# Kernel optimization log

Measured on AMD Instinct MI355X. Metric: run time of the kernel, lower is better.

Reference implementation:

```python
import jax, jax.numpy as jnp
import numpy as np

N_NODES = 100000
N_EDGES = 3200000
D_IN = 256
D_OUT = 256


def setup_inputs() -> dict:
    key = jax.random.key(0)
    k1, k2, k3, k4, k5 = jax.random.split(key, 5)
    inputs = jax.random.normal(k1, (N_NODES, D_IN), dtype=jnp.float32)
    adj_row = jax.random.randint(k2, (N_EDGES,), 0, N_NODES, dtype=jnp.int32)
    adj_col = jax.random.randint(k3, (N_EDGES,), 0, N_NODES, dtype=jnp.int32)
    adj_val = jax.random.uniform(k4, (N_EDGES,), dtype=jnp.float32)
    # xavier-uniform init for weight, zeros for bias (as in reset_parameters)
    limit = float(np.sqrt(6.0 / (D_IN + D_OUT)))
    weight = jax.random.uniform(k5, (D_IN, D_OUT), dtype=jnp.float32,
                                minval=-limit, maxval=limit)
    bias = jnp.zeros((D_OUT,), dtype=jnp.float32)
    return {"inputs": inputs, "adj_row": adj_row, "adj_col": adj_col,
            "adj_val": adj_val, "weight": weight, "bias": bias}


def reference(inputs, adj_row, adj_col, adj_val, weight, bias) -> jnp.ndarray:
    # support = X @ W  -> [N, D_OUT]
    support = inputs @ weight
    # SpMM: out[r] = sum_{e: row[e]==r} val[e] * support[col[e]]
    gathered = support[adj_col] * adj_val[:, None]          # [E, D_OUT]
    output = jax.ops.segment_sum(gathered, adj_row, num_segments=N_NODES)
    return output + bias
```

## Files before the change

### kernel.cpp

```cpp
#include <hip/hip_runtime.h>

#define N_NODES 100000
#define N_EDGES 3200000
#define D 256
#define GEMM_TILES (N_NODES / 32)
#define GEMM_BLOCKS ((GEMM_TILES + 3) / 4)
#define WSH_BLOCKS 32

#define RPB 16
#define NB_BUCKETS (N_NODES / RPB)
#define NBLK_B ((NB_BUCKETS + 255) / 256)
#define P2_CAP 4096

#define HIST_P 256
#define EDGES_PER_HB (N_EDGES / HIST_P)

using u16 = unsigned short;
using u32 = unsigned int;

typedef __attribute__((ext_vector_type(8))) short bf16x8;
typedef __attribute__((ext_vector_type(4))) float f32x4;

__device__ inline u16 f2bf(float f) {
    u32 x = __builtin_bit_cast(u32, f);
    return (u16)((x + 0x7FFFu + ((x >> 16) & 1u)) >> 16);
}
__device__ inline float bf2f(u16 u) {
    return __builtin_bit_cast(float, (u32)u << 16);
}

__global__ __launch_bounds__(256) void prep_kernel(
    const float* __restrict__ W, u16* __restrict__ Wf)
{
    const int t = blockIdx.x * 256 + threadIdx.x;
    const int kt = t >> 10;
    const int nt = (t >> 6) & 15;
    const int lane = t & 63;
    const int kbase = kt * 32 + ((lane >> 4) * 8);
    const int n = nt * 16 + (lane & 15);
    u16 frag[8];
    #pragma unroll
    for (int j = 0; j < 8; ++j)
        frag[j] = f2bf(W[(size_t)(kbase + j) * D + n]);
    #pragma unroll
    for (int j = 0; j < 8; ++j)
        Wf[(size_t)t * 8 + j] = frag[j];
}

__global__ __launch_bounds__(256) void gemm_kernel(
    const float* __restrict__ X, const u16* __restrict__ Wf,
    u16* __restrict__ S)
{
    const int lane = threadIdx.x & 63;
    const int tile = blockIdx.x * 4 + (threadIdx.x >> 6);
    if (tile >= GEMM_TILES) return;
    const int row0 = tile * 32;
    const int m = lane & 15;
    const int quad = lane >> 4;

    f32x4 acc0[16], acc1[16];
    #pragma unroll
    for (int t = 0; t < 16; ++t) {
        acc0[t] = (f32x4){0.f, 0.f, 0.f, 0.f};
        acc1[t] = (f32x4){0.f, 0.f, 0.f, 0.f};
    }

    const float* xA = X + (size_t)(row0 + m) * D + quad * 8;
    const float* xB = X + (size_t)(row0 + 16 + m) * D + quad * 8;
    const bf16x8* __restrict__ Bf = (const bf16x8*)Wf;

    for (int k0 = 0; k0 < 8; ++k0) {
        const float4 a0l = *(const float4*)(xA + k0 * 32);
        const float4 a0h = *(const float4*)(xA + k0 * 32 + 4);
        const float4 a1l = *(const float4*)(xB + k0 * 32);
        const float4 a1h = *(const float4*)(xB + k0 * 32 + 4);
        bf16x8 a0, a1;
        a0[0] = (short)f2bf(a0l.x); a0[1] = (short)f2bf(a0l.y);
        a0[2] = (short)f2bf(a0l.z); a0[3] = (short)f2bf(a0l.w);
        a0[4] = (short)f2bf(a0h.x); a0[5] = (short)f2bf(a0h.y);
        a0[6] = (short)f2bf(a0h.z); a0[7] = (short)f2bf(a0h.w);
        a1[0] = (short)f2bf(a1l.x); a1[1] = (short)f2bf(a1l.y);
        a1[2] = (short)f2bf(a1l.z); a1[3] = (short)f2bf(a1l.w);
        a1[4] = (short)f2bf(a1h.x); a1[5] = (short)f2bf(a1h.y);
        a1[6] = (short)f2bf(a1h.z); a1[7] = (short)f2bf(a1h.w);

        const bf16x8* bp = Bf + (size_t)k0 * 1024 + lane;
        #pragma unroll
        for (int g = 0; g < 4; ++g) {
            const bf16x8 b0 = bp[g * 256 + 0];
            const bf16x8 b1 = bp[g * 256 + 64];
            const bf16x8 b2 = bp[g * 256 + 128];
            const bf16x8 b3 = bp[g * 256 + 192];
            acc0[g*4+0] = __builtin_amdgcn_mfma_f32_16x16x32_bf16(a0, b0, acc0[g*4+0], 0, 0, 0);
            acc1[g*4+0] = __builtin_amdgcn_mfma_f32_16x16x32_bf16(a1, b0, acc1[g*4+0], 0, 0, 0);
            acc0[g*4+1] = __builtin_amdgcn_mfma_f32_16x16x32_bf16(a0, b1, acc0[g*4+1], 0, 0, 0);
            acc1[g*4+1] = __builtin_amdgcn_mfma_f32_16x16x32_bf16(a1, b1, acc1[g*4+1], 0, 0, 0);
            acc0[g*4+2] = __builtin_amdgcn_mfma_f32_16x16x32_bf16(a0, b2, acc0[g*4+2], 0, 0, 0);
            acc1[g*4+2] = __builtin_amdgcn_mfma_f32_16x16x32_bf16(a1, b2, acc1[g*4+2], 0, 0, 0);
            acc0[g*4+3] = __builtin_amdgcn_mfma_f32_16x16x32_bf16(a0, b3, acc0[g*4+3], 0, 0, 0);
            acc1[g*4+3] = __builtin_amdgcn_mfma_f32_16x16x32_bf16(a1, b3, acc1[g*4+3], 0, 0, 0);
        }
    }

    #pragma unroll
    for (int nt = 0; nt < 16; ++nt) {
        u16* Sp = S + (size_t)(nt >> 3) * ((size_t)N_NODES * 128);
        const int cip = (nt & 7) * 16 + m;
        #pragma unroll
        for (int i = 0; i < 4; ++i) {
            Sp[(size_t)(row0 + quad * 4 + i) * 128 + cip]      = f2bf(acc0[nt][i]);
            Sp[(size_t)(row0 + 16 + quad * 4 + i) * 128 + cip] = f2bf(acc1[nt][i]);
        }
    }
}

__global__ __launch_bounds__(1024) void hist_kernel(
    const int* __restrict__ row, u32* __restrict__ hglob)
{
    __shared__ u32 h[NB_BUCKETS];
    const int tid = threadIdx.x;
    for (int j = tid; j < NB_BUCKETS; j += 1024) h[j] = 0u;
    __syncthreads();
    const int e0 = blockIdx.x * EDGES_PER_HB;
    for (int i = tid; i < EDGES_PER_HB; i += 1024)
        atomicAdd(&h[row[e0 + i] >> 4], 1u);
    __syncthreads();
    u32* dst = hglob + (size_t)blockIdx.x * NB_BUCKETS;
    for (int j = tid; j < NB_BUCKETS; j += 1024) dst[j] = h[j];
}

__global__ __launch_bounds__(256) void colsum_kernel(
    const u32* __restrict__ hglob, u32* __restrict__ tot, int* __restrict__ bsum)
{
    __shared__ int sh[4];
    const int b = blockIdx.x * 256 + threadIdx.x;
    u32 s = 0u;
    if (b < NB_BUCKETS) {
        #pragma unroll 8
        for (int p = 0; p < HIST_P; ++p)
            s += hglob[(size_t)p * NB_BUCKETS + b];
        tot[b] = s;
    }
    int x = (int)s;
    #pragma unroll
    for (int off = 32; off > 0; off >>= 1) x += __shfl_xor(x, off);
    if ((threadIdx.x & 63) == 0) sh[threadIdx.x >> 6] = x;
    __syncthreads();
    if (threadIdx.x == 0) bsum[blockIdx.x] = sh[0] + sh[1] + sh[2] + sh[3];
}

__global__ __launch_bounds__(64) void bscan_kernel(
    const int* __restrict__ bsum, int* __restrict__ boff,
    int* __restrict__ starts, int* __restrict__ bstart)
{
    const int tid = threadIdx.x;
    const int c = (tid < NBLK_B) ? bsum[tid] : 0;
    int x = c;
    #pragma unroll
    for (int off = 1; off < 64; off <<= 1) {
        int y = __shfl_up(x, off);
        if (tid >= off) x += y;
    }
    if (tid < NBLK_B) boff[tid] = x - c;
    if (tid == 0) {
        starts[N_NODES] = N_EDGES;
        bstart[NB_BUCKETS] = N_EDGES;
    }
}

__global__ __launch_bounds__(256) void blocalscan_kernel(
    const u32* __restrict__ tot, const int* __restrict__ boff,
    int* __restrict__ bstart, int* __restrict__ bcur)
{
    __shared__ int wsum[4];
    const int tid = threadIdx.x, lane = tid & 63, wv = tid >> 6;
    const int i = blockIdx.x * 256 + tid;
    const int c = (i < NB_BUCKETS) ? (int)tot[i] : 0;
    int x = c;
    #pragma unroll
    for (int off = 1; off < 64; off <<= 1) {
        int y = __shfl_up(x, off);
        if (lane >= off) x += y;
    }
    if (lane == 63) wsum[wv] = x;
    __syncthreads();
    if (tid == 0) {
        int run = 0;
        #pragma unroll
        for (int w = 0; w < 4; ++w) { int t = wsum[w]; wsum[w] = run; run += t; }
    }
    __syncthreads();
    const int excl = x - c + wsum[wv] + boff[blockIdx.x];
    if (i < NB_BUCKETS) { bstart[i] = excl; bcur[i] = excl; }
}

__global__ __launch_bounds__(256) void binplace_kernel(
    const int* __restrict__ row, const int* __restrict__ col,
    const float* __restrict__ val, int* __restrict__ bcur,
    uint2* __restrict__ pce)
{
    const int e = blockIdx.x * 256 + threadIdx.x;
    const int r = row[e];
    const u32 c = (u32)col[e];
    const float v = val[e];
    const int pos = atomicAdd(&bcur[r / RPB], 1);
    pce[pos] = make_uint2(c | ((u32)(r & (RPB - 1)) << 17),
                          __builtin_bit_cast(u32, v));
}

__global__ __launch_bounds__(256) void bucketsort_kernel(
    const int* __restrict__ bstart, uint2* __restrict__ pce,
    int* __restrict__ starts)
{
    __shared__ uint2 ent[P2_CAP];
    __shared__ int rcnt[RPB];
    __shared__ int rcur[RPB];
    const int b = blockIdx.x;
    const int tid = threadIdx.x;
    const int base = bstart[b];
    const int n = bstart[b + 1] - base;
    if (tid < RPB) rcnt[tid] = 0;
    __syncthreads();
    for (int i = tid; i < n; i += 256) ent[i] = pce[base + i];
    __syncthreads();
    for (int i = tid; i < n; i += 256)
        atomicAdd(&rcnt[(ent[i].x >> 17) & (RPB - 1)], 1);
    __syncthreads();
    if (tid == 0) {
        int run = 0;
        #pragma unroll
        for (int j = 0; j < RPB; ++j) { rcur[j] = run; run += rcnt[j]; }
    }
    __syncthreads();
    if (tid < RPB) starts[b * RPB + tid] = base + rcur[tid];
    __syncthreads();
    for (int i = tid; i < n; i += 256) {
        const uint2 e = ent[i];
        const int rl = (int)((e.x >> 17) & (u32)(RPB - 1));
        const int pos = atomicAdd(&rcur[rl], 1);
        pce[base + pos] = make_uint2(e.x & 0x1FFFFu, e.y);
    }
}

__global__ __launch_bounds__(256) void reduce_kernel(
    const u16* __restrict__ S, const int* __restrict__ starts,
    const uint2* __restrict__ pce, const float* __restrict__ bias,
    float* __restrict__ out, int plane)
{
    const int lane = threadIdx.x & 63;
    const int r = blockIdx.x * 4 + (threadIdx.x >> 6);
    const int s0 = starts[r];
    const int s1 = starts[r + 1];

    const u32* __restrict__ Sp =
        (const u32*)(S + (size_t)plane * ((size_t)N_NODES * 128));
    float2 acc = make_float2(0.f, 0.f);

    for (int base = s0; base < s1; base += 64) {
        const int n = min(64, s1 - base);
        uint2 pr = make_uint2(0u, 0u);
        if (lane < n) pr = pce[base + lane];
        const int c = (int)pr.x;
        const float v = __builtin_bit_cast(float, pr.y);

        int i = 0;
        for (; i + 8 <= n; i += 8) {
            int cc[8]; float vv[8]; u32 s[8];
            #pragma unroll
            for (int u = 0; u < 8; ++u) {
                cc[u] = __shfl(c, i + u);
                vv[u] = __shfl(v, i + u);
            }
            #pragma unroll
            for (int u = 0; u < 8; ++u)
                s[u] = Sp[(size_t)cc[u] * 64 + lane];
            #pragma unroll
            for (int u = 0; u < 8; ++u) {
                acc.x += vv[u] * bf2f((u16)(s[u] & 0xFFFFu));
                acc.y += vv[u] * bf2f((u16)(s[u] >> 16));
            }
        }
        for (; i < n; ++i) {
            const int c0 = __shfl(c, i);
            const float v0 = __shfl(v, i);
            const u32 a0 = Sp[(size_t)c0 * 64 + lane];
            acc.x += v0 * bf2f((u16)(a0 & 0xFFFFu));
            acc.y += v0 * bf2f((u16)(a0 >> 16));
        }
    }

    const float2 b2 = ((const float2*)bias)[plane * 64 + lane];
    acc.x += b2.x; acc.y += b2.y;
    ((float2*)out)[(size_t)r * 128 + plane * 64 + lane] = acc;
}

extern "C" void kernel_launch(void* const* d_in, const int* in_sizes, int n_in,
                              void* d_out, int out_size, void* d_ws, size_t ws_size,
                              hipStream_t stream) {
    const float* X    = (const float*)d_in[0];
    const int*   row  = (const int*)d_in[1];
    const int*   col  = (const int*)d_in[2];
    const float* val  = (const float*)d_in[3];
    const float* W    = (const float*)d_in[4];
    const float* bias = (const float*)d_in[5];
    float* out = (float*)d_out;

    char* ws = (char*)d_ws;
    u16*   Sx     = (u16*)ws;
    int*   starts = (int*)(ws + 51200000);
    uint2* pce    = (uint2*)(ws + 51600064);
    u16*   Wf     = (u16*)(ws + 77200064);
    u32*   hglob  = (u32*)(ws + 77331136);
    u32*   tot    = (u32*)(ws + 83731136);
    int*   bsum   = (int*)(ws + 83756736);
    int*   boff   = (int*)(ws + 83757760);
    int*   bstart = (int*)(ws + 83758784);
    int*   bcur   = (int*)(ws + 83784384);

    prep_kernel<<<WSH_BLOCKS, 256, 0, stream>>>(W, Wf);

    gemm_kernel<<<GEMM_BLOCKS, 256, 0, stream>>>(X, Wf, Sx);

    hist_kernel<<<HIST_P, 1024, 0, stream>>>(row, hglob);
    colsum_kernel<<<NBLK_B, 256, 0, stream>>>(hglob, tot, bsum);
    bscan_kernel<<<1, 64, 0, stream>>>(bsum, boff, starts, bstart);
    blocalscan_kernel<<<NBLK_B, 256, 0, stream>>>(tot, boff, bstart, bcur);

    binplace_kernel<<<N_EDGES / 256, 256, 0, stream>>>(row, col, val, bcur, pce);
    bucketsort_kernel<<<NB_BUCKETS, 256, 0, stream>>>(bstart, pce, starts);

    reduce_kernel<<<N_NODES / 4, 256, 0, stream>>>(Sx, starts, pce, bias, out, 0);
    reduce_kernel<<<N_NODES / 4, 256, 0, stream>>>(Sx, starts, pce, bias, out, 1);
}
```

Baseline: 623.9 us.

## Replace global-atomic bucket placement with per-block partitioned counting sort

Sorting edges by row now uses 64-row bins and 128 partition blocks. Each partition's histogram is turned into per-partition offsets, so the scatter uses shared-memory atomic cursors instead of global atomics on bucket counters. The scan pipeline is cut to fewer kernels, and the bin sort now handles 64 rows per bin with a wave-level scan. The risk is fewer, larger blocks in the scatter stage (only 128 blocks), which may underuse the GPU, and bins near the 4096-entry shared capacity.

```diff
diff --git a/kernel.cpp b/kernel.cpp
--- a/kernel.cpp
+++ b/kernel.cpp
@@ -7,13 +7,12 @@
 #define GEMM_BLOCKS ((GEMM_TILES + 3) / 4)
 #define WSH_BLOCKS 32
 
-#define RPB 16
-#define NB_BUCKETS (N_NODES / RPB)
-#define NBLK_B ((NB_BUCKETS + 255) / 256)
-#define P2_CAP 4096
-
-#define HIST_P 256
-#define EDGES_PER_HB (N_EDGES / HIST_P)
+#define BIN_SHIFT 6
+#define BIN_ROWS 64
+#define NBIN 1563
+#define P1 128
+#define EPP (N_EDGES / P1)
+#define BSORT_CAP 4096
 
 using u16 = unsigned short;
 using u32 = unsigned int;
@@ -114,131 +113,127 @@
     }
 }
 
-__global__ __launch_bounds__(1024) void hist_kernel(
-    const int* __restrict__ row, u32* __restrict__ hglob)
-{
-    __shared__ u32 h[NB_BUCKETS];
+__global__ __launch_bounds__(512) void hist2_kernel(
+    const int* __restrict__ row, u32* __restrict__ hcnt)
+{
+    __shared__ u32 h[NBIN];
     const int tid = threadIdx.x;
-    for (int j = tid; j < NB_BUCKETS; j += 1024) h[j] = 0u;
-    __syncthreads();
-    const int e0 = blockIdx.x * EDGES_PER_HB;
-    for (int i = tid; i < EDGES_PER_HB; i += 1024)
-        atomicAdd(&h[row[e0 + i] >> 4], 1u);
-    __syncthreads();
-    u32* dst = hglob + (size_t)blockIdx.x * NB_BUCKETS;
-    for (int j = tid; j < NB_BUCKETS; j += 1024) dst[j] = h[j];
-}
-
-__global__ __launch_bounds__(256) void colsum_kernel(
-    const u32* __restrict__ hglob, u32* __restrict__ tot, int* __restrict__ bsum)
-{
-    __shared__ int sh[4];
-    const int b = blockIdx.x * 256 + threadIdx.x;
-    u32 s = 0u;
-    if (b < NB_BUCKETS) {
-        #pragma unroll 8
-        for (int p = 0; p < HIST_P; ++p)
-            s += hglob[(size_t)p * NB_BUCKETS + b];
-        tot[b] = s;
-    }
-    int x = (int)s;
-    #pragma unroll
-    for (int off = 32; off > 0; off >>= 1) x += __shfl_xor(x, off);
-    if ((threadIdx.x & 63) == 0) sh[threadIdx.x >> 6] = x;
-    __syncthreads();
-    if (threadIdx.x == 0) bsum[blockIdx.x] = sh[0] + sh[1] + sh[2] + sh[3];
-}
-
-__global__ __launch_bounds__(64) void bscan_kernel(
-    const int* __restrict__ bsum, int* __restrict__ boff,
-    int* __restrict__ starts, int* __restrict__ bstart)
-{
-    const int tid = threadIdx.x;
-    const int c = (tid < NBLK_B) ? bsum[tid] : 0;
-    int x = c;
-    #pragma unroll
-    for (int off = 1; off < 64; off <<= 1) {
-        int y = __shfl_up(x, off);
-        if (tid >= off) x += y;
-    }
-    if (tid < NBLK_B) boff[tid] = x - c;
-    if (tid == 0) {
-        starts[N_NODES] = N_EDGES;
-        bstart[NB_BUCKETS] = N_EDGES;
-    }
-}
-
-__global__ __launch_bounds__(256) void blocalscan_kernel(
-    const u32* __restrict__ tot, const int* __restrict__ boff,
-    int* __restrict__ bstart, int* __restrict__ bcur)
-{
-    __shared__ int wsum[4];
+    const int p = blockIdx.x;
+    for (int j = tid; j < NBIN; j += 512) h[j] = 0u;
+    __syncthreads();
+    const int e0 = p * EPP;
+    for (int i = tid; i < EPP; i += 512)
+        atomicAdd(&h[row[e0 + i] >> BIN_SHIFT], 1u);
+    __syncthreads();
+    u32* dst = hcnt + (size_t)p * NBIN;
+    for (int j = tid; j < NBIN; j += 512) dst[j] = h[j];
+}
+
+__global__ __launch_bounds__(128) void binoffsets_kernel(
+    u32* __restrict__ hcnt, u32* __restrict__ coltot)
+{
+    __shared__ int w0tot;
+    const int b = blockIdx.x;
     const int tid = threadIdx.x, lane = tid & 63, wv = tid >> 6;
-    const int i = blockIdx.x * 256 + tid;
-    const int c = (i < NB_BUCKETS) ? (int)tot[i] : 0;
+    const int c = (int)hcnt[(size_t)tid * NBIN + b];
     int x = c;
     #pragma unroll
     for (int off = 1; off < 64; off <<= 1) {
         int y = __shfl_up(x, off);
         if (lane >= off) x += y;
     }
-    if (lane == 63) wsum[wv] = x;
-    __syncthreads();
+    if (tid == 63) w0tot = x;
+    __syncthreads();
+    const int excl = x - c + (wv ? w0tot : 0);
+    hcnt[(size_t)tid * NBIN + b] = (u32)excl;
+    if (tid == 127) coltot[b] = (u32)(excl + c);
+}
+
+__global__ __launch_bounds__(64) void binscan_kernel(
+    const u32* __restrict__ coltot, int* __restrict__ binstart,
+    int* __restrict__ starts)
+{
+    const int tid = threadIdx.x;
+    int carry = 0;
+    for (int ch = 0; ch < (NBIN + 63) / 64; ++ch) {
+        const int idx = ch * 64 + tid;
+        const int c = (idx < NBIN) ? (int)coltot[idx] : 0;
+        int x = c;
+        #pragma unroll
+        for (int off = 1; off < 64; off <<= 1) {
+            int y = __shfl_up(x, off);
+            if (tid >= off) x += y;
+        }
+        if (idx < NBIN) binstart[idx] = carry + x - c;
+        carry += __shfl(x, 63);
+    }
     if (tid == 0) {
-        int run = 0;
-        #pragma unroll
-        for (int w = 0; w < 4; ++w) { int t = wsum[w]; wsum[w] = run; run += t; }
-    }
-    __syncthreads();
-    const int excl = x - c + wsum[wv] + boff[blockIdx.x];
-    if (i < NB_BUCKETS) { bstart[i] = excl; bcur[i] = excl; }
-}
-
-__global__ __launch_bounds__(256) void binplace_kernel(
+        binstart[NBIN] = N_EDGES;
+        starts[N_NODES] = N_EDGES;
+    }
+}
+
+__global__ __launch_bounds__(512) void scatter1_kernel(
     const int* __restrict__ row, const int* __restrict__ col,
-    const float* __restrict__ val, int* __restrict__ bcur,
-    uint2* __restrict__ pce)
-{
-    const int e = blockIdx.x * 256 + threadIdx.x;
-    const int r = row[e];
-    const u32 c = (u32)col[e];
-    const float v = val[e];
-    const int pos = atomicAdd(&bcur[r / RPB], 1);
-    pce[pos] = make_uint2(c | ((u32)(r & (RPB - 1)) << 17),
-                          __builtin_bit_cast(u32, v));
-}
-
-__global__ __launch_bounds__(256) void bucketsort_kernel(
-    const int* __restrict__ bstart, uint2* __restrict__ pce,
+    const float* __restrict__ val, const u32* __restrict__ poff,
+    const int* __restrict__ binstart, uint2* __restrict__ pce)
+{
+    __shared__ int lcur[NBIN];
+    const int tid = threadIdx.x;
+    const int p = blockIdx.x;
+    for (int b = tid; b < NBIN; b += 512)
+        lcur[b] = binstart[b] + (int)poff[(size_t)p * NBIN + b];
+    __syncthreads();
+    const int e0 = p * EPP;
+    for (int i = tid; i < EPP; i += 512) {
+        const int e = e0 + i;
+        const int r = row[e];
+        const u32 c = (u32)col[e];
+        const float v = val[e];
+        const int pos = atomicAdd(&lcur[r >> BIN_SHIFT], 1);
+        pce[pos] = make_uint2(c | ((u32)(r & (BIN_ROWS - 1)) << 17),
+                              __builtin_bit_cast(u32, v));
+    }
+}
+
+__global__ __launch_bounds__(256) void binsort_kernel(
+    const int* __restrict__ binstart, uint2* __restrict__ pce,
     int* __restrict__ starts)
 {
-    __shared__ uint2 ent[P2_CAP];
-    __shared__ int rcnt[RPB];
-    __shared__ int rcur[RPB];
+    __shared__ uint2 ent[BSORT_CAP];
+    __shared__ int rcnt[BIN_ROWS];
+    __shared__ int rcur[BIN_ROWS];
     const int b = blockIdx.x;
     const int tid = threadIdx.x;
-    const int base = bstart[b];
-    const int n = bstart[b + 1] - base;
-    if (tid < RPB) rcnt[tid] = 0;
-    __syncthreads();
-    for (int i = tid; i < n; i += 256) ent[i] = pce[base + i];
-    __syncthreads();
-    for (int i = tid; i < n; i += 256)
-        atomicAdd(&rcnt[(ent[i].x >> 17) & (RPB - 1)], 1);
-    __syncthreads();
-    if (tid == 0) {
-        int run = 0;
+    const int base = binstart[b];
+    const int n = binstart[b + 1] - base;
+    if (tid < BIN_ROWS) rcnt[tid] = 0;
+    __syncthreads();
+    for (int i = tid; i < n; i += 256) {
+        const uint2 e = pce[base + i];
+        ent[i] = e;
+        atomicAdd(&rcnt[(e.x >> 17) & (BIN_ROWS - 1)], 1);
+    }
+    __syncthreads();
+    if (tid < BIN_ROWS) {
+        const int c = rcnt[tid];
+        int x = c;
         #pragma unroll
-        for (int j = 0; j < RPB; ++j) { rcur[j] = run; run += rcnt[j]; }
-    }
-    __syncthreads();
-    if (tid < RPB) starts[b * RPB + tid] = base + rcur[tid];
+        for (int off = 1; off < 64; off <<= 1) {
+            int y = __shfl_up(x, off);
+            if (tid >= off) x += y;
+        }
+        const int excl = x - c;
+        rcur[tid] = excl;
+        const int r = b * BIN_ROWS + tid;
+        if (r < N_NODES) starts[r] = base + excl;
+    }
     __syncthreads();
     for (int i = tid; i < n; i += 256) {
         const uint2 e = ent[i];
-        const int rl = (int)((e.x >> 17) & (u32)(RPB - 1));
-        const int pos = atomicAdd(&rcur[rl], 1);
-        pce[base + pos] = make_uint2(e.x & 0x1FFFFu, e.y);
+        const int rl = (int)((e.x >> 17) & (u32)(BIN_ROWS - 1));
+        const int pos = base + atomicAdd(&rcur[rl], 1);
+        pce[pos] = make_uint2(e.x & 0x1FFFFu, e.y);
     }
 }
 
@@ -306,28 +301,24 @@
     float* out = (float*)d_out;
 
     char* ws = (char*)d_ws;
-    u16*   Sx     = (u16*)ws;
-    int*   starts = (int*)(ws + 51200000);
-    uint2* pce    = (uint2*)(ws + 51600064);
-    u16*   Wf     = (u16*)(ws + 77200064);
-    u32*   hglob  = (u32*)(ws + 77331136);
-    u32*   tot    = (u32*)(ws + 83731136);
-    int*   bsum   = (int*)(ws + 83756736);
-    int*   boff   = (int*)(ws + 83757760);
-    int*   bstart = (int*)(ws + 83758784);
-    int*   bcur   = (int*)(ws + 83784384);
+    u16*   Sx      = (u16*)ws;
+    int*   starts  = (int*)(ws + 51200000);
+    uint2* pce     = (uint2*)(ws + 51600064);
+    u16*   Wf      = (u16*)(ws + 77200064);
+    u32*   hcnt    = (u32*)(ws + 77331136);
+    u32*   coltot  = (u32*)(ws + 78131392);
+    int*   binstart= (int*)(ws + 78137664);
 
     prep_kernel<<<WSH_BLOCKS, 256, 0, stream>>>(W, Wf);
 
     gemm_kernel<<<GEMM_BLOCKS, 256, 0, stream>>>(X, Wf, Sx);
 
-    hist_kernel<<<HIST_P, 1024, 0, stream>>>(row, hglob);
-    colsum_kernel<<<NBLK_B, 256, 0, stream>>>(hglob, tot, bsum);
-    bscan_kernel<<<1, 64, 0, stream>>>(bsum, boff, starts, bstart);
-    blocalscan_kernel<<<NBLK_B, 256, 0, stream>>>(tot, boff, bstart, bcur);
-
-    binplace_kernel<<<N_EDGES / 256, 256, 0, stream>>>(row, col, val, bcur, pce);
-    bucketsort_kernel<<<NB_BUCKETS, 256, 0, stream>>>(bstart, pce, starts);
+    hist2_kernel<<<P1, 512, 0, stream>>>(row, hcnt);
+    binoffsets_kernel<<<NBIN, 128, 0, stream>>>(hcnt, coltot);
+    binscan_kernel<<<1, 64, 0, stream>>>(coltot, binstart, starts);
+
+    scatter1_kernel<<<P1, 512, 0, stream>>>(row, col, val, hcnt, binstart, pce);
+    binsort_kernel<<<NBIN, 256, 0, stream>>>(binstart, pce, starts);
 
     reduce_kernel<<<N_NODES / 4, 256, 0, stream>>>(Sx, starts, pce, bias, out, 0);
     reduce_kernel<<<N_NODES / 4, 256, 0, stream>>>(Sx, starts, pce, bias, out, 1);
```

After: 588.1 us. -5.7%, faster.
